# Kernel optimization log

Hardware: AMD Instinct MI355X
Metric: run time of the kernel (lower is better)

Reference implementation:

```python
import jax, jax.numpy as jnp
import numpy as np

B, T_DEC, F = 16, 32, 8
S_ENC, H, L = 256, 512, 2
TGT_IDX = jnp.arange(8)  # target_indices = all features


def setup_inputs() -> dict:
    key = jax.random.key(0)
    ks = jax.random.split(key, 16)
    g = lambda k, shp, s=0.05: jax.random.normal(k, shp, dtype=jnp.float32) * s
    return {
        'target': jax.random.normal(ks[0], (B, T_DEC, F), dtype=jnp.float32),
        'hidden0': jax.random.normal(ks[1], (L, B, H), dtype=jnp.float32),
        'enc_outputs': jax.random.normal(ks[2], (B, S_ENC, H), dtype=jnp.float32),
        # Attention params
        'attn_W': g(ks[3], (H, 2 * H)), 'attn_b': jnp.zeros((H,), jnp.float32),
        'v_w': g(ks[4], (H,)),
        # GRU layer 0 (input = F + H) and layer 1 (input = H); PyTorch layout [3H, in]
        'gru_Wih0': g(ks[5], (3 * H, F + H)), 'gru_Whh0': g(ks[6], (3 * H, H)),
        'gru_bih0': jnp.zeros((3 * H,), jnp.float32), 'gru_bhh0': jnp.zeros((3 * H,), jnp.float32),
        'gru_Wih1': g(ks[7], (3 * H, H)), 'gru_Whh1': g(ks[8], (3 * H, H)),
        'gru_bih1': jnp.zeros((3 * H,), jnp.float32), 'gru_bhh1': jnp.zeros((3 * H,), jnp.float32),
        # output Linear (2H + F -> F)
        'out_W': g(ks[9], (F, 2 * H + F)), 'out_b': jnp.zeros((F,), jnp.float32),
        'input_seq_len': S_ENC,
    }


def _gru_cell(x, h, Wih, Whh, bih, bhh):
    # PyTorch GRUCell math; gate order [r, z, n]
    gi = x @ Wih.T + bih
    gh = h @ Whh.T + bhh
    ir, iz, inn = jnp.split(gi, 3, axis=-1)
    hr, hz, hn = jnp.split(gh, 3, axis=-1)
    r = jax.nn.sigmoid(ir + hr)
    z = jax.nn.sigmoid(iz + hz)
    n = jnp.tanh(inn + r * hn)
    return (1.0 - z) * n + z * h


def reference(target, hidden0, enc_outputs, attn_W, attn_b, v_w,
              gru_Wih0, gru_Whh0, gru_bih0, gru_bhh0,
              gru_Wih1, gru_Whh1, gru_bih1, gru_bhh1,
              out_W, out_b, input_seq_len):
    b, s, h = enc_outputs.shape

    def step(carry, target_t):
        hidden, x_in = carry  # hidden [L,B,H], x_in [B,F]
        h_top = hidden[-1]
        # Bahdanau attention
        hid_rep = jnp.broadcast_to(h_top[:, None, :], (b, s, h))
        energy = jnp.tanh(jnp.concatenate([hid_rep, enc_outputs], axis=-1) @ attn_W.T + attn_b)
        scores = energy @ v_w  # [B,S]
        weightings = jax.nn.softmax(scores, axis=1)
        weighted = jnp.einsum('bs,bsh->bh', weightings, enc_outputs)  # [B,H]
        # stacked GRU single step
        x = jnp.concatenate([x_in, weighted], axis=-1)  # [B, F+H]
        h0 = _gru_cell(x, hidden[0], gru_Wih0, gru_Whh0, gru_bih0, gru_bhh0)
        h1 = _gru_cell(h0, hidden[1], gru_Wih1, gru_Whh1, gru_bih1, gru_bhh1)
        new_hidden = jnp.stack([h0, h1])
        # output projection + relu (applied in DecoderBase.forward)
        out = jnp.concatenate([h1, weighted, x_in], axis=-1) @ out_W.T + out_b
        out = jax.nn.relu(out)  # [B,F]
        # no teacher forcing (teacher_force_prob=None): replace target features with prediction
        next_in = target_t.at[:, TGT_IDX].set(out)
        return (new_hidden, next_in), out

    target_ts = jnp.swapaxes(target, 0, 1)  # [T,B,F]
    (_, _), outs = jax.lax.scan(step, (hidden0, target[:, 0, :]), target_ts)
    return jnp.swapaxes(outs, 0, 1)  # [B,T,F]
```

## Files before the change

### kernel.cpp

```cpp
#include <hip/hip_runtime.h>


namespace {
constexpr int NTHR = 256, NBLK = 256;

constexpr int OFF_HIDPS = 8192;
constexpr int OFF_WNS   = 16384;
constexpr int OFF_LS    = 81920;
constexpr int OFF_H0S   = 82176;
constexpr int OFF_H1S   = 86272;
constexpr int OFF_AEH   = 90368;
constexpr int OFF_WHID  = OFF_AEH + 131072;
constexpr int OFF_WIH0  = OFF_WHID + 131072;
constexpr int OFF_WHH0  = OFF_WIH0 + 399360;
constexpr int OFF_WIH1  = OFF_WHH0 + 393216;
constexpr int OFF_WHH1  = OFF_WIH1 + 393216;
constexpr int OFF_ENCP  = OFF_WHH1 + 393216;

constexpr int L_H1   = 0;
constexpr int L_H0   = 256;
constexpr int L_HIDP = 512;
constexpr int L_ES   = 1024;
constexpr int L_HX   = 1040;
constexpr int L_AX   = 1304;
constexpr int L_AH   = 1400;
constexpr int L_BIH0 = 1496, L_BHH0 = 1592, L_BIH1 = 1688, L_BHH1 = 1784;
constexpr int L_VW   = 1880;
constexpr int L_XINL = 2392;
constexpr int L_LL   = 2400;
constexpr int LDS_FLOATS = 8192;
}

typedef _Float16 h2 __attribute__((ext_vector_type(2)));
union U32H { unsigned u; h2 h; };

__device__ __forceinline__ float dot2(unsigned a, unsigned b, float acc) {
    U32H ua, ub; ua.u = a; ub.u = b;
#if __has_builtin(__builtin_amdgcn_fdot2)
    return __builtin_amdgcn_fdot2(ua.h, ub.h, acc, false);
#else
    return acc + (float)ua.h.x * (float)ub.h.x + (float)ua.h.y * (float)ub.h.y;
#endif
}
__device__ __forceinline__ unsigned packh2(float a, float b) {
    U32H u; u.h = h2{(_Float16)a, (_Float16)b}; return u.u;
}
__device__ __forceinline__ float fsig(float x) { return 1.0f / (1.0f + __expf(-x)); }
__device__ __forceinline__ float ftanhf(float x) {
    float e = __expf(2.0f * x);
    return 1.0f - 2.0f / (e + 1.0f);
}
__device__ __forceinline__ float cload(const float* p) {
    return __hip_atomic_load(p, __ATOMIC_RELAXED, __HIP_MEMORY_SCOPE_SYSTEM);
}
__device__ __forceinline__ void cstore(float* p, float v) {
    __hip_atomic_store(p, v, __ATOMIC_RELAXED, __HIP_MEMORY_SCOPE_SYSTEM);
}
__device__ __forceinline__ unsigned ucload(const unsigned* p) {
    return __hip_atomic_load(p, __ATOMIC_RELAXED, __HIP_MEMORY_SCOPE_SYSTEM);
}
__device__ __forceinline__ void ucstore(unsigned* p, unsigned v) {
    __hip_atomic_store(p, v, __ATOMIC_RELAXED, __HIP_MEMORY_SCOPE_SYSTEM);
}

__device__ __forceinline__ void bar_sync_flush(unsigned* cnt, unsigned target) {
    __syncthreads();
    if (threadIdx.x == 0) {
        __builtin_amdgcn_fence(__ATOMIC_RELEASE, "agent");
        __hip_atomic_fetch_add(cnt, 1u, __ATOMIC_RELAXED, __HIP_MEMORY_SCOPE_SYSTEM);
        while (__hip_atomic_load(cnt, __ATOMIC_RELAXED, __HIP_MEMORY_SCOPE_SYSTEM) < target)
            __builtin_amdgcn_s_sleep(8);
        __builtin_amdgcn_fence(__ATOMIC_ACQUIRE, "agent");
    }
    __syncthreads();
}

__global__ __launch_bounds__(NTHR) void decoder_kernel(
    const float* __restrict__ target, const float* __restrict__ hidden0,
    const float* __restrict__ enc, const float* __restrict__ attn_W,
    const float* __restrict__ attn_b, const float* __restrict__ v_w,
    const float* __restrict__ Wih0, const float* __restrict__ Whh0,
    const float* __restrict__ bih0, const float* __restrict__ bhh0,
    const float* __restrict__ Wih1, const float* __restrict__ Whh1,
    const float* __restrict__ bih1, const float* __restrict__ bhh1,
    const float* __restrict__ outW, const float* __restrict__ outBias,
    float* __restrict__ out, float* __restrict__ ws) {
    const int tid = threadIdx.x, bid = blockIdx.x;
    const int b = bid >> 4, s = bid & 15;
    unsigned* tags = (unsigned*)ws;
    unsigned* gridCnt = (unsigned*)ws + 8180;

    float* hidPS = ws + OFF_HIDPS;
    unsigned* wnS = (unsigned*)(ws + OFF_WNS);
    float* lS = ws + OFF_LS;
    unsigned* h0S = (unsigned*)(ws + OFF_H0S);
    unsigned* h1S = (unsigned*)(ws + OFF_H1S);
    unsigned* aehU  = (unsigned*)(ws + OFF_AEH);
    unsigned* whidU = (unsigned*)(ws + OFF_WHID);
    unsigned* wih0U = (unsigned*)(ws + OFF_WIH0);
    unsigned* whh0U = (unsigned*)(ws + OFF_WHH0);
    unsigned* wih1U = (unsigned*)(ws + OFF_WIH1);
    unsigned* whh1U = (unsigned*)(ws + OFF_WHH1);
    unsigned* encpU = (unsigned*)(ws + OFF_ENCP);

    __shared__ __align__(16) float lds[LDS_FLOATS];
    unsigned* ldsU = (unsigned*)lds;
    const int gtid = bid * NTHR + tid;

    for (int i = gtid; i < 131072; i += NBLK * NTHR) {
        const int jr = i >> 8, p = i & 255;
        aehU[i]  = packh2(attn_W[jr * 1024 + 512 + 2 * p], attn_W[jr * 1024 + 513 + 2 * p]);
        whidU[i] = packh2(attn_W[jr * 1024 + 2 * p], attn_W[jr * 1024 + 1 + 2 * p]);
    }
    for (int i = gtid; i < 399360; i += NBLK * NTHR)
        wih0U[i] = packh2(Wih0[2 * i], Wih0[2 * i + 1]);
    for (int i = gtid; i < 393216; i += NBLK * NTHR) {
        whh0U[i] = packh2(Whh0[2 * i], Whh0[2 * i + 1]);
        wih1U[i] = packh2(Wih1[2 * i], Wih1[2 * i + 1]);
        whh1U[i] = packh2(Whh1[2 * i], Whh1[2 * i + 1]);
    }
    bar_sync_flush(gridCnt, NBLK);

    {
        for (int i = 0; i < 32; ++i) {
            const int idx = tid + i * 256;
            lds[idx] = enc[(b * 256 + s * 16) * 512 + idx];
        }
        __syncthreads();
        float a0[16], a1[16];
        const float bb0 = attn_b[2 * tid], bb1 = attn_b[2 * tid + 1];
#pragma unroll
        for (int sl = 0; sl < 16; ++sl) { a0[sl] = bb0; a1[sl] = bb1; }
        const unsigned* w0 = &aehU[(2 * tid) * 256];
        const unsigned* w1 = &aehU[(2 * tid + 1) * 256];
        for (int p = 0; p < 256; ++p) {
            const unsigned ww0 = w0[p], ww1 = w1[p];
#pragma unroll
            for (int sl = 0; sl < 16; ++sl) {
                const unsigned epk = packh2(lds[sl * 512 + 2 * p], lds[sl * 512 + 2 * p + 1]);
                a0[sl] = dot2(epk, ww0, a0[sl]);
                a1[sl] = dot2(epk, ww1, a1[sl]);
            }
        }
        for (int sl = 0; sl < 16; ++sl)
            encpU[(b * 256 + s * 16 + sl) * 256 + tid] = packh2(a0[sl], a1[sl]);
        __syncthreads();
    }

    if (tid < 96) {
        const int grow = (tid >> 5) * 512 + s * 32 + (tid & 31);
        lds[L_BIH0 + tid] = bih0[grow]; lds[L_BHH0 + tid] = bhh0[grow];
        lds[L_BIH1 + tid] = bih1[grow]; lds[L_BHH1 + tid] = bhh1[grow];
    }
    lds[L_VW + tid] = v_w[tid];
    lds[L_VW + 256 + tid] = v_w[256 + tid];
    __syncthreads();

    ldsU[L_H1 + tid] = packh2(hidden0[8192 + b * 512 + 2 * tid],
                              hidden0[8192 + b * 512 + 2 * tid + 1]);
    ldsU[L_H0 + tid] = packh2(hidden0[b * 512 + 2 * tid], hidden0[b * 512 + 2 * tid + 1]);
    if (tid < 8) lds[L_XINL + tid] = target[b * 256 + tid];
    if (tid < 4) ldsU[L_HX + 260 + tid] = 0u;
    __syncthreads();

    for (int t = 0; t < 32; ++t) {
        const unsigned tgt = (unsigned)(t + 1);

        {
            const int r = tid >> 3, sub = tid & 7;
            const uint4* wrow = (const uint4*)&whidU[(s * 32 + r) * 256 + sub * 32];
            const uint4* h1p = (const uint4*)&ldsU[L_H1 + sub * 32];
            float acc = 0.f;
#pragma unroll
            for (int k4 = 0; k4 < 8; ++k4) {
                const uint4 hv = h1p[k4], wv = wrow[k4];
                acc = dot2(hv.x, wv.x, acc); acc = dot2(hv.y, wv.y, acc);
                acc = dot2(hv.z, wv.z, acc); acc = dot2(hv.w, wv.w, acc);
            }
            acc += __shfl_down(acc, 4, 8); acc += __shfl_down(acc, 2, 8); acc += __shfl_down(acc, 1, 8);
            if (sub == 0) cstore(&hidPS[(b * 16 + s) * 32 + r], acc);
        }
        __syncthreads();
        if (tid == 0) ucstore(&tags[(b * 16 + s) * 32 + 0], tgt);
        if (tid < 16) {
            const unsigned* tg = &tags[(b * 16 + tid) * 32 + 0];
            while (ucload(tg) < tgt) __builtin_amdgcn_s_sleep(1);
        }
        __syncthreads();
        __builtin_amdgcn_fence(__ATOMIC_ACQUIRE, "workgroup");
        lds[L_HIDP + tid] = cload(&hidPS[(b * 16 + (tid >> 5)) * 32 + (tid & 31)]);
        lds[L_HIDP + 256 + tid] = cload(&hidPS[(b * 16 + 8 + (tid >> 5)) * 32 + (tid & 31)]);
        __syncthreads();

        {
            const int sloc = tid >> 4, sub = tid & 15;
            const unsigned* ep = &encpU[(b * 256 + s * 16 + sloc) * 256];
            float acc = 0.f;
#pragma unroll 4
            for (int k2 = 0; k2 < 16; ++k2) {
                const int p = k2 * 16 + sub;
                U32H u; u.u = ep[p];
                acc += lds[L_VW + 2 * p] * ftanhf((float)u.h.x + lds[L_HIDP + 2 * p]);
                acc += lds[L_VW + 2 * p + 1] * ftanhf((float)u.h.y + lds[L_HIDP + 2 * p + 1]);
            }
            acc += __shfl_down(acc, 8, 16); acc += __shfl_down(acc, 4, 16);
            acc += __shfl_down(acc, 2, 16); acc += __shfl_down(acc, 1, 16);
            if (sub == 0) lds[L_ES + sloc] = __expf(acc);
        }
        __syncthreads();
        {
            float l = 0.f;
#pragma unroll
            for (int i = 0; i < 16; ++i) l += lds[L_ES + i];
            const float invl = 1.f / l;
            float wp0 = 0.f, wp1 = 0.f;
            const float2* er = (const float2*)&enc[(b * 256 + s * 16) * 512];
#pragma unroll
            for (int sl = 0; sl < 16; ++sl) {
                const float2 e = er[sl * 256 + tid];
                const float es = lds[L_ES + sl];
                wp0 += es * e.x; wp1 += es * e.y;
            }
            ucstore(&wnS[(b * 16 + s) * 256 + tid], packh2(wp0 * invl, wp1 * invl));
            if (tid == 0) cstore(&lS[b * 16 + s], l);
        }
        __syncthreads();
        if (tid == 0) ucstore(&tags[(b * 16 + s) * 32 + 1], tgt);
        if (tid < 16) {
            const unsigned* tg = &tags[(b * 16 + tid) * 32 + 1];
            while (ucload(tg) < tgt) __builtin_amdgcn_s_sleep(1);
            lds[L_LL + tid] = cload(&lS[b * 16 + tid]);
        }
        __syncthreads();
        __builtin_amdgcn_fence(__ATOMIC_ACQUIRE, "workgroup");
        {
            float Lsum = 0.f;
#pragma unroll
            for (int i = 0; i < 16; ++i) Lsum += lds[L_LL + i];
            const float inv = 1.f / Lsum;
            float w0 = 0.f, w1 = 0.f;
#pragma unroll
            for (int sp = 0; sp < 16; ++sp) {
                U32H u; u.u = ucload(&wnS[(b * 16 + sp) * 256 + tid]);
                const float Ls = lds[L_LL + sp];
                w0 += Ls * (float)u.h.x; w1 += Ls * (float)u.h.y;
            }
            ldsU[L_HX + 4 + tid] = packh2(w0 * inv, w1 * inv);
            if (tid < 4)
                ldsU[L_HX + tid] = packh2(lds[L_XINL + 2 * tid], lds[L_XINL + 2 * tid + 1]);
        }
        __syncthreads();

        if (tid < 192) {
            const int u = tid >> 1, sub = tid & 1;
            const int gh = u >> 5, r = u & 31;
            const int grow = gh * 512 + s * 32 + r;
            const uint4* wx = (const uint4*)&wih0U[grow * 260 + sub * 132];
            const uint4* xp = (const uint4*)&ldsU[L_HX + sub * 132];
            float ax = 0.f;
#pragma unroll 11
            for (int k4 = 0; k4 < 33; ++k4) {
                const uint4 xv = xp[k4], wv = wx[k4];
                ax = dot2(xv.x, wv.x, ax); ax = dot2(xv.y, wv.y, ax);
                ax = dot2(xv.z, wv.z, ax); ax = dot2(xv.w, wv.w, ax);
            }
            const uint4* wh = (const uint4*)&whh0U[grow * 256 + sub * 128];
            const uint4* hp = (const uint4*)&ldsU[L_H0 + sub * 128];
            float ah = 0.f;
#pragma unroll 8
            for (int k4 = 0; k4 < 32; ++k4) {
                const uint4 hv = hp[k4], wv = wh[k4];
                ah = dot2(hv.x, wv.x, ah); ah = dot2(hv.y, wv.y, ah);
                ah = dot2(hv.z, wv.z, ah); ah = dot2(hv.w, wv.w, ah);
            }
            ax += __shfl_down(ax, 1, 2); ah += __shfl_down(ah, 1, 2);
            if (sub == 0) {
                lds[L_AX + u] = ax + lds[L_BIH0 + u];
                lds[L_AH + u] = ah + lds[L_BHH0 + u];
            }
        }
        __syncthreads();
        if (tid < 32) {
            const int r = tid;
            const float rg = fsig(lds[L_AX + r] + lds[L_AH + r]);
            const float z = fsig(lds[L_AX + 32 + r] + lds[L_AH + 32 + r]);
            const float n = ftanhf(lds[L_AX + 64 + r] + rg * lds[L_AH + 64 + r]);
            U32H u; u.u = ldsU[L_H0 + s * 16 + (r >> 1)];
            const float hold = (r & 1) ? (float)u.h.y : (float)u.h.x;
            const float hs = (1.f - z) * n + z * hold;
            const float hsn = __shfl_down(hs, 1, 2);
            if ((r & 1) == 0)
                ucstore(&h0S[(b * 16 + s) * 16 + (r >> 1)], packh2(hs, hsn));
        }
        __syncthreads();
        if (tid == 0) ucstore(&tags[(b * 16 + s) * 32 + 2], tgt);
        if (tid < 16) {
            const unsigned* tg = &tags[(b * 16 + tid) * 32 + 2];
            while (ucload(tg) < tgt) __builtin_amdgcn_s_sleep(1);
        }
        __syncthreads();
        __builtin_amdgcn_fence(__ATOMIC_ACQUIRE, "workgroup");
        ldsU[L_H0 + tid] = ucload(&h0S[(b * 16 + (tid >> 4)) * 16 + (tid & 15)]);
        __syncthreads();

        if (tid < 192) {
            const int u = tid >> 1, sub = tid & 1;
            const int gh = u >> 5, r = u & 31;
            const int grow = gh * 512 + s * 32 + r;
            const uint4* wx = (const uint4*)&wih1U[grow * 256 + sub * 128];
            const uint4* xp = (const uint4*)&ldsU[L_H0 + sub * 128];
            float ax = 0.f;
#pragma unroll 8
            for (int k4 = 0; k4 < 32; ++k4) {
                const uint4 xv = xp[k4], wv = wx[k4];
                ax = dot2(xv.x, wv.x, ax); ax = dot2(xv.y, wv.y, ax);
                ax = dot2(xv.z, wv.z, ax); ax = dot2(xv.w, wv.w, ax);
            }
            const uint4* wh = (const uint4*)&whh1U[grow * 256 + sub * 128];
            const uint4* hp = (const uint4*)&ldsU[L_H1 + sub * 128];
            float ah = 0.f;
#pragma unroll 8
            for (int k4 = 0; k4 < 32; ++k4) {
                const uint4 hv = hp[k4], wv = wh[k4];
                ah = dot2(hv.x, wv.x, ah); ah = dot2(hv.y, wv.y, ah);
                ah = dot2(hv.z, wv.z, ah); ah = dot2(hv.w, wv.w, ah);
            }
            ax += __shfl_down(ax, 1, 2); ah += __shfl_down(ah, 1, 2);
            if (sub == 0) {
                lds[L_AX + u] = ax + lds[L_BIH1 + u];
                lds[L_AH + u] = ah + lds[L_BHH1 + u];
            }
        }
        __syncthreads();
        if (tid < 32) {
            const int r = tid;
            const float rg = fsig(lds[L_AX + r] + lds[L_AH + r]);
            const float z = fsig(lds[L_AX + 32 + r] + lds[L_AH + 32 + r]);
            const float n = ftanhf(lds[L_AX + 64 + r] + rg * lds[L_AH + 64 + r]);
            U32H u; u.u = ldsU[L_H1 + s * 16 + (r >> 1)];
            const float hold = (r & 1) ? (float)u.h.y : (float)u.h.x;
            const float hs = (1.f - z) * n + z * hold;
            const float hsn = __shfl_down(hs, 1, 2);
            if ((r & 1) == 0)
                ucstore(&h1S[(b * 16 + s) * 16 + (r >> 1)], packh2(hs, hsn));
        }
        __syncthreads();
        if (tid == 0) ucstore(&tags[(b * 16 + s) * 32 + 3], tgt);
        if (tid < 16) {
            const unsigned* tg = &tags[(b * 16 + tid) * 32 + 3];
            while (ucload(tg) < tgt) __builtin_amdgcn_s_sleep(1);
        }
        __syncthreads();
        __builtin_amdgcn_fence(__ATOMIC_ACQUIRE, "workgroup");
        ldsU[L_H1 + tid] = ucload(&h1S[(b * 16 + (tid >> 4)) * 16 + (tid & 15)]);
        __syncthreads();

        {
            const int f = tid >> 5, l = tid & 31;
            const float* ow = &outW[f * 1032];
            float acc = 0.f;
#pragma unroll
            for (int i = 0; i < 8; ++i) {
                const int k2 = i * 32 + l;
                U32H u; u.u = ldsU[L_H1 + k2];
                acc += ow[2 * k2] * (float)u.h.x + ow[2 * k2 + 1] * (float)u.h.y;
            }
#pragma unroll
            for (int i = 0; i < 8; ++i) {
                const int k2 = i * 32 + l;
                U32H u; u.u = ldsU[L_HX + 4 + k2];
                acc += ow[512 + 2 * k2] * (float)u.h.x + ow[512 + 2 * k2 + 1] * (float)u.h.y;
            }
            if (l < 8) acc += ow[1024 + l] * lds[L_XINL + l];
            acc += __shfl_down(acc, 16, 32); acc += __shfl_down(acc, 8, 32);
            acc += __shfl_down(acc, 4, 32); acc += __shfl_down(acc, 2, 32);
            acc += __shfl_down(acc, 1, 32);
            if (l == 0) {
                const float o = fmaxf(acc + outBias[f], 0.f);
                lds[L_ES + f] = o;
                if (s == 0) out[b * 256 + t * 8 + f] = o;
            }
        }
        __syncthreads();
        if (tid < 8) lds[L_XINL + tid] = lds[L_ES + tid];
        __syncthreads();
    }
}

extern "C" void kernel_launch(void* const* d_in, const int* in_sizes, int n_in,
                              void* d_out, int out_size, void* d_ws, size_t ws_size,
                              hipStream_t stream) {
    (void)in_sizes; (void)n_in; (void)out_size; (void)ws_size;
    hipMemsetAsync(d_ws, 0, 32768, stream);
    decoder_kernel<<<NBLK, NTHR, 0, stream>>>(
        (const float*)d_in[0], (const float*)d_in[1], (const float*)d_in[2],
        (const float*)d_in[3], (const float*)d_in[4], (const float*)d_in[5],
        (const float*)d_in[6], (const float*)d_in[7], (const float*)d_in[8],
        (const float*)d_in[9], (const float*)d_in[10], (const float*)d_in[11],
        (const float*)d_in[12], (const float*)d_in[13], (const float*)d_in[14],
        (const float*)d_in[15], (float*)d_out, (float*)d_ws);
}
```

Measured before the change: 882.1 us.

## Fuse attention hidden projection into GRU layer-1 step to drop a grid barrier

The per-step attention projection of the top hidden state (W_hid·h1) previously ran as its own phase at the start of each step, with a cross-block tag barrier. Now each block computes partial projections from its own 32 new h1 values using a transposed fp16 weight copy. It publishes these partials alongside h1 and reduces all 16 partials after the existing h1 barrier. This removes one inter-block synchronisation per timestep, at the cost of more global partial-sum traffic (512 floats per block) and a one-time prologue computing the initial projection.

```diff
diff --git a/kernel.cpp b/kernel.cpp
--- a/kernel.cpp
+++ b/kernel.cpp
@@ -4,18 +4,18 @@
 namespace {
 constexpr int NTHR = 256, NBLK = 256;
 
-constexpr int OFF_HIDPS = 8192;
-constexpr int OFF_WNS   = 16384;
-constexpr int OFF_LS    = 81920;
-constexpr int OFF_H0S   = 82176;
-constexpr int OFF_H1S   = 86272;
-constexpr int OFF_AEH   = 90368;
-constexpr int OFF_WHID  = OFF_AEH + 131072;
-constexpr int OFF_WIH0  = OFF_WHID + 131072;
-constexpr int OFF_WHH0  = OFF_WIH0 + 399360;
-constexpr int OFF_WIH1  = OFF_WHH0 + 393216;
-constexpr int OFF_WHH1  = OFF_WIH1 + 393216;
-constexpr int OFF_ENCP  = OFF_WHH1 + 393216;
+constexpr int OFF_WNS   = 8192;
+constexpr int OFF_LS    = 73728;
+constexpr int OFF_H0S   = 73984;
+constexpr int OFF_H1S   = 78080;
+constexpr int OFF_HPP   = 82176;
+constexpr int OFF_AEH   = 213248;
+constexpr int OFF_WHIDT = 344320;
+constexpr int OFF_WIH0  = 475392;
+constexpr int OFF_WHH0  = 874752;
+constexpr int OFF_WIH1  = 1267968;
+constexpr int OFF_WHH1  = 1661184;
+constexpr int OFF_ENCP  = 2054400;
 
 constexpr int L_H1   = 0;
 constexpr int L_H0   = 256;
@@ -28,6 +28,7 @@
 constexpr int L_VW   = 1880;
 constexpr int L_XINL = 2392;
 constexpr int L_LL   = 2400;
+constexpr int L_H1S  = 2416;
 constexpr int LDS_FLOATS = 8192;
 }
 
@@ -90,13 +91,13 @@
     unsigned* tags = (unsigned*)ws;
     unsigned* gridCnt = (unsigned*)ws + 8180;
 
-    float* hidPS = ws + OFF_HIDPS;
     unsigned* wnS = (unsigned*)(ws + OFF_WNS);
     float* lS = ws + OFF_LS;
     unsigned* h0S = (unsigned*)(ws + OFF_H0S);
     unsigned* h1S = (unsigned*)(ws + OFF_H1S);
-    unsigned* aehU  = (unsigned*)(ws + OFF_AEH);
-    unsigned* whidU = (unsigned*)(ws + OFF_WHID);
+    float* hPP = ws + OFF_HPP;
+    unsigned* aehU   = (unsigned*)(ws + OFF_AEH);
+    unsigned* whidTU = (unsigned*)(ws + OFF_WHIDT);
     unsigned* wih0U = (unsigned*)(ws + OFF_WIH0);
     unsigned* whh0U = (unsigned*)(ws + OFF_WHH0);
     unsigned* wih1U = (unsigned*)(ws + OFF_WIH1);
@@ -109,8 +110,11 @@
 
     for (int i = gtid; i < 131072; i += NBLK * NTHR) {
         const int jr = i >> 8, p = i & 255;
-        aehU[i]  = packh2(attn_W[jr * 1024 + 512 + 2 * p], attn_W[jr * 1024 + 513 + 2 * p]);
-        whidU[i] = packh2(attn_W[jr * 1024 + 2 * p], attn_W[jr * 1024 + 1 + 2 * p]);
+        aehU[i] = packh2(attn_W[jr * 1024 + 512 + 2 * p], attn_W[jr * 1024 + 513 + 2 * p]);
+    }
+    for (int i = gtid; i < 131072; i += NBLK * NTHR) {
+        const int kp = i >> 9, r = i & 511;
+        whidTU[i] = packh2(attn_W[r * 1024 + 2 * kp], attn_W[r * 1024 + 2 * kp + 1]);
     }
     for (int i = gtid; i < 399360; i += NBLK * NTHR)
         wih0U[i] = packh2(Wih0[2 * i], Wih0[2 * i + 1]);
@@ -163,34 +167,37 @@
     if (tid < 4) ldsU[L_HX + 260 + tid] = 0u;
     __syncthreads();
 
+    {
+        float p0 = 0.f, p1 = 0.f;
+#pragma unroll
+        for (int k = 0; k < 16; ++k) {
+            const unsigned hp = ldsU[L_H1 + s * 16 + k];
+            p0 = dot2(whidTU[(s * 16 + k) * 512 + tid], hp, p0);
+            p1 = dot2(whidTU[(s * 16 + k) * 512 + 256 + tid], hp, p1);
+        }
+        cstore(&hPP[(b * 16 + s) * 512 + tid], p0);
+        cstore(&hPP[(b * 16 + s) * 512 + 256 + tid], p1);
+        __syncthreads();
+        if (tid == 0) ucstore(&tags[(b * 16 + s) * 32 + 0], 1u);
+        if (tid < 16) {
+            const unsigned* tg = &tags[(b * 16 + tid) * 32 + 0];
+            while (ucload(tg) < 1u) __builtin_amdgcn_s_sleep(1);
+        }
+        __syncthreads();
+        __builtin_amdgcn_fence(__ATOMIC_ACQUIRE, "workgroup");
+        float a0 = 0.f, a1 = 0.f;
+#pragma unroll
+        for (int sp = 0; sp < 16; ++sp) {
+            a0 += cload(&hPP[(b * 16 + sp) * 512 + tid]);
+            a1 += cload(&hPP[(b * 16 + sp) * 512 + 256 + tid]);
+        }
+        lds[L_HIDP + tid] = a0;
+        lds[L_HIDP + 256 + tid] = a1;
+        __syncthreads();
+    }
+
     for (int t = 0; t < 32; ++t) {
         const unsigned tgt = (unsigned)(t + 1);
-
-        {
-            const int r = tid >> 3, sub = tid & 7;
-            const uint4* wrow = (const uint4*)&whidU[(s * 32 + r) * 256 + sub * 32];
-            const uint4* h1p = (const uint4*)&ldsU[L_H1 + sub * 32];
-            float acc = 0.f;
-#pragma unroll
-            for (int k4 = 0; k4 < 8; ++k4) {
-                const uint4 hv = h1p[k4], wv = wrow[k4];
-                acc = dot2(hv.x, wv.x, acc); acc = dot2(hv.y, wv.y, acc);
-                acc = dot2(hv.z, wv.z, acc); acc = dot2(hv.w, wv.w, acc);
-            }
-            acc += __shfl_down(acc, 4, 8); acc += __shfl_down(acc, 2, 8); acc += __shfl_down(acc, 1, 8);
-            if (sub == 0) cstore(&hidPS[(b * 16 + s) * 32 + r], acc);
-        }
-        __syncthreads();
-        if (tid == 0) ucstore(&tags[(b * 16 + s) * 32 + 0], tgt);
-        if (tid < 16) {
-            const unsigned* tg = &tags[(b * 16 + tid) * 32 + 0];
-            while (ucload(tg) < tgt) __builtin_amdgcn_s_sleep(1);
-        }
-        __syncthreads();
-        __builtin_amdgcn_fence(__ATOMIC_ACQUIRE, "workgroup");
-        lds[L_HIDP + tid] = cload(&hidPS[(b * 16 + (tid >> 5)) * 32 + (tid & 31)]);
-        lds[L_HIDP + 256 + tid] = cload(&hidPS[(b * 16 + 8 + (tid >> 5)) * 32 + (tid & 31)]);
-        __syncthreads();
 
         {
             const int sloc = tid >> 4, sub = tid & 15;
@@ -341,8 +348,23 @@
             const float hold = (r & 1) ? (float)u.h.y : (float)u.h.x;
             const float hs = (1.f - z) * n + z * hold;
             const float hsn = __shfl_down(hs, 1, 2);
-            if ((r & 1) == 0)
-                ucstore(&h1S[(b * 16 + s) * 16 + (r >> 1)], packh2(hs, hsn));
+            if ((r & 1) == 0) {
+                const unsigned pk = packh2(hs, hsn);
+                ldsU[L_H1S + (r >> 1)] = pk;
+                ucstore(&h1S[(b * 16 + s) * 16 + (r >> 1)], pk);
+            }
+        }
+        __syncthreads();
+        {
+            float p0 = 0.f, p1 = 0.f;
+#pragma unroll
+            for (int k = 0; k < 16; ++k) {
+                const unsigned hp = ldsU[L_H1S + k];
+                p0 = dot2(whidTU[(s * 16 + k) * 512 + tid], hp, p0);
+                p1 = dot2(whidTU[(s * 16 + k) * 512 + 256 + tid], hp, p1);
+            }
+            cstore(&hPP[(b * 16 + s) * 512 + tid], p0);
+            cstore(&hPP[(b * 16 + s) * 512 + 256 + tid], p1);
         }
         __syncthreads();
         if (tid == 0) ucstore(&tags[(b * 16 + s) * 32 + 3], tgt);
@@ -353,6 +375,16 @@
         __syncthreads();
         __builtin_amdgcn_fence(__ATOMIC_ACQUIRE, "workgroup");
         ldsU[L_H1 + tid] = ucload(&h1S[(b * 16 + (tid >> 4)) * 16 + (tid & 15)]);
+        {
+            float a0 = 0.f, a1 = 0.f;
+#pragma unroll
+            for (int sp = 0; sp < 16; ++sp) {
+                a0 += cload(&hPP[(b * 16 + sp) * 512 + tid]);
+                a1 += cload(&hPP[(b * 16 + sp) * 512 + 256 + tid]);
+            }
+            lds[L_HIDP + tid] = a0;
+            lds[L_HIDP + 256 + tid] = a1;
+        }
         __syncthreads();
 
         {
```

Result: slower. 1.332 ms (+51.1%).
